# Optimization experiments

Hardware: AMD Instinct MI355X
Metric: run time of the kernel (lower is better)

Reference implementation:

```python
import jax, jax.numpy as jnp
import numpy as np

BETA = 20.0  # Softplus beta in the original torch module
# upper-triangular (offset=1) indices of a 3x3 matrix, matching torch.triu_indices(3,3,1)
TRIU_R = np.array([0, 0, 1])
TRIU_C = np.array([1, 2, 2])


def _softplus(x):
    # torch.nn.Softplus(beta=20): log(1+exp(beta*x))/beta, numerically stable via jax.nn.softplus
    return jax.nn.softplus(BETA * x) / BETA


def setup_inputs() -> dict:
    key = jax.random.key(0)
    ks = jax.random.split(key, 9)
    N = 1_000_000
    h = 32

    def lin_init(k, fan_in, fan_out):
        bound = 1.0 / np.sqrt(fan_in)
        kw, kb = jax.random.split(k)
        W = jax.random.uniform(kw, (fan_in, fan_out), jnp.float32, -bound, bound)
        b = jax.random.uniform(kb, (fan_out,), jnp.float32, -bound, bound)
        return W, b

    x = jax.random.normal(ks[0], (N, 3), jnp.float32)
    W1, b1 = lin_init(ks[1], 3, h)
    W2, b2 = lin_init(ks[2], h, h)
    W3, b3 = lin_init(ks[3], h, h)
    W4, b4 = lin_init(ks[4], h, 3)
    return {"x": x, "W1": W1, "b1": b1, "W2": W2, "b2": b2,
            "W3": W3, "b3": b3, "W4": W4, "b4": b4}


def reference(x, W1, b1, W2, b2, W3, b3, W4, b4):
    def mlp(p):  # p: [3] -> [3] (the 3 free entries of the antisymmetric matrix)
        h = _softplus(p @ W1 + b1)
        h = _softplus(h @ W2 + b2)
        h = _softplus(h @ W3 + b3)
        return h @ W4 + b4

    def pres_A(p):  # p: [3] -> antisymmetric [3,3]
        v = mlp(p)
        M = jnp.zeros((3, 3), dtype=p.dtype).at[TRIU_R, TRIU_C].set(v)
        return M - M.T

    # per-sample Jacobian dA/dx: [N, 3, 3, 3]
    J = jax.vmap(jax.jacrev(pres_A))(x.reshape(-1, 3))
    # trace over (column, x-dim): out[n, a] = sum_i dA[n, a, i]/dx[n, i]
    return jnp.einsum('naii->na', J)
```

## Files before the change

### kernel.cpp

```cpp
#include <hip/hip_runtime.h>
#include <math.h>

#define NTHR 256
#define WAVES_PER_BLOCK 4

typedef __attribute__((ext_vector_type(8))) _Float16 f16x8;
typedef __attribute__((ext_vector_type(2))) _Float16 half2v;
typedef __attribute__((ext_vector_type(4))) float f32x4;
typedef __attribute__((ext_vector_type(4))) unsigned uint4v;

#define CEXP 28.85390082f
#define KLOG 0.03465735903f

#define EXP2F(v) __builtin_amdgcn_exp2f(v)
#define LOG2F(v) __builtin_amdgcn_logf(v)

static __device__ __forceinline__ f32x4 splat4(float v) { return (f32x4){v, v, v, v}; }

static __device__ __forceinline__ void act_hs4(f32x4 z, f32x4& h, f32x4& s) {
    f32x4 az = __builtin_elementwise_abs(splat4(CEXP) * z);
    f32x4 e;
    #pragma unroll
    for (int i = 0; i < 4; ++i) e[i] = EXP2F(-az[i]);
    f32x4 p = splat4(1.0f) + e;
    f32x4 l;
    #pragma unroll
    for (int i = 0; i < 4; ++i) l[i] = LOG2F(p[i]);
    f32x4 zp = __builtin_elementwise_max(z, splat4(0.0f));
    f32x4 q  = __builtin_elementwise_fma(splat4(-CEXP), zp, -l);
    f32x4 t;
    #pragma unroll
    for (int i = 0; i < 4; ++i) t[i] = EXP2F(q[i]);
    s = splat4(1.0f) - t;
    h = __builtin_elementwise_fma(splat4(KLOG), l, zp);
}

static __device__ __forceinline__ f32x4 sigmoid4(f32x4 z) {
    f32x4 cz = splat4(-CEXP) * z;
    f32x4 e;
    #pragma unroll
    for (int i = 0; i < 4; ++i) e[i] = EXP2F(cz[i]);
    f32x4 p = splat4(1.0f) + e;
    f32x4 r;
    #pragma unroll
    for (int i = 0; i < 4; ++i) r[i] = __builtin_amdgcn_rcpf(p[i]);
    return r;
}

static __device__ __forceinline__ unsigned pk(float a, float b) {
    return __builtin_bit_cast(unsigned, __builtin_amdgcn_cvt_pkrtz(a, b));
}

static __device__ __forceinline__ f16x8 pack8v(const f32x4& a, const f32x4& b) {
    uint4v u = {pk(a[0], a[1]), pk(a[2], a[3]), pk(b[0], b[1]), pk(b[2], b[3])};
    return __builtin_bit_cast(f16x8, u);
}
static __device__ __forceinline__ void fsplit8v(const f32x4& a, const f32x4& b,
                                                f16x8& hi, f16x8& lo) {
    unsigned h[4], l[4];
    #pragma unroll
    for (int p2 = 0; p2 < 2; ++p2) {
        float u0 = a[2 * p2], u1 = a[2 * p2 + 1];
        unsigned hp = pk(u0, u1);
        half2v hh = __builtin_bit_cast(half2v, hp);
        h[p2] = hp;
        l[p2] = pk(u0 - (float)hh[0], u1 - (float)hh[1]);
        float w0 = b[2 * p2], w1 = b[2 * p2 + 1];
        unsigned hq = pk(w0, w1);
        half2v hh2 = __builtin_bit_cast(half2v, hq);
        h[2 + p2] = hq;
        l[2 + p2] = pk(w0 - (float)hh2[0], w1 - (float)hh2[1]);
    }
    hi = __builtin_bit_cast(f16x8, (uint4v){h[0], h[1], h[2], h[3]});
    lo = __builtin_bit_cast(f16x8, (uint4v){l[0], l[1], l[2], l[3]});
}

static __device__ __forceinline__ f32x4 mfma2f(f16x8 w, f16x8 bh, f16x8 bl, f32x4 c) {
    c = __builtin_amdgcn_mfma_f32_16x16x32_f16(w, bh, c, 0, 0, 0);
    c = __builtin_amdgcn_mfma_f32_16x16x32_f16(w, bl, c, 0, 0, 0);
    return c;
}
static __device__ __forceinline__ f32x4 mfma1t(f16x8 w, f16x8 b, f32x4 c) {
    return __builtin_amdgcn_mfma_f32_16x16x32_f16(w, b, c, 0, 0, 0);
}

__global__ void __launch_bounds__(NTHR)
presdiv_kernel(const float* __restrict__ x,
               const float* __restrict__ W1, const float* __restrict__ b1,
               const float* __restrict__ W2, const float* __restrict__ b2,
               const float* __restrict__ W3, const float* __restrict__ b3,
               const float* __restrict__ W4,
               float* __restrict__ out, int N)
{
    const int lane = threadIdx.x & 63;
    const int wid  = threadIdx.x >> 6;
    const int n16  = lane & 15;
    const int g    = lane >> 4;

    f16x8 w2[2], w3[2];
    #pragma unroll
    for (int h = 0; h < 2; ++h) {
        #pragma unroll
        for (int j = 0; j < 8; ++j) {
            const int k2 = g * 8 + j;
            w2[h][j] = (_Float16)W2[k2 * 32 + 16 * h + n16];
            const int k3 = (j < 4) ? (4 * g + j) : (16 + 4 * g + (j - 4));
            w3[h][j] = (_Float16)W3[k3 * 32 + 16 * h + n16];
        }
    }
    f32x4 w1v[3][2], bb1v[2];
    #pragma unroll
    for (int c = 0; c < 2; ++c)
        #pragma unroll
        for (int i = 0; i < 4; ++i) {
            const int j = 4 * c + i;
            bb1v[c][i] = b1[g * 8 + j];
            #pragma unroll
            for (int d = 0; d < 3; ++d) w1v[d][c][i] = W1[d * 32 + g * 8 + j];
        }
    f32x4 bb2v[2], bb3v[2], w4c[2][3];
    #pragma unroll
    for (int h = 0; h < 2; ++h)
        #pragma unroll
        for (int r = 0; r < 4; ++r) {
            const int row = 16 * h + 4 * g + r;
            bb2v[h][r] = b2[row];
            bb3v[h][r] = b3[row];
            #pragma unroll
            for (int k = 0; k < 3; ++k) w4c[h][k][r] = W4[row * 3 + k];
        }

    const int ntiles = (N + 15) >> 4;
    const int nwaves = gridDim.x * WAVES_PER_BLOCK;
    const f32x4 vzero = {0.f, 0.f, 0.f, 0.f};

    for (int tile = blockIdx.x * WAVES_PER_BLOCK + wid; tile < ntiles; tile += nwaves) {
        int s = tile * 16 + n16;
        if (s >= N) s = N - 1;
        const f32x4 X0 = splat4(x[3 * s + 0]);
        const f32x4 X1 = splat4(x[3 * s + 1]);
        const f32x4 X2 = splat4(x[3 * s + 2]);

        f32x4 vFv[2], v0v[2], v1v[2], v2v[2];
        #pragma unroll
        for (int c = 0; c < 2; ++c) {
            f32x4 z = __builtin_elementwise_fma(X0, w1v[0][c], bb1v[c]);
            z = __builtin_elementwise_fma(X1, w1v[1][c], z);
            z = __builtin_elementwise_fma(X2, w1v[2][c], z);
            f32x4 hv, sv;
            act_hs4(z, hv, sv);
            vFv[c] = hv;
            v0v[c] = sv * w1v[0][c];
            v1v[c] = sv * w1v[1][c];
            v2v[c] = sv * w1v[2][c];
        }

        f32x4 aF[2], a0[2], a1[2], a2[2];
        aF[0] = bb2v[0]; aF[1] = bb2v[1];
        a0[0] = a0[1] = a1[0] = a1[1] = a2[0] = a2[1] = vzero;

        f16x8 bh, bl;
        fsplit8v(vFv[0], vFv[1], bh, bl);
        aF[0] = mfma2f(w2[0], bh, bl, aF[0]);
        aF[1] = mfma2f(w2[1], bh, bl, aF[1]);
        f16x8 tb = pack8v(v0v[0], v0v[1]);
        a0[0] = mfma1t(w2[0], tb, a0[0]);
        a0[1] = mfma1t(w2[1], tb, a0[1]);
        tb = pack8v(v1v[0], v1v[1]);
        a1[0] = mfma1t(w2[0], tb, a1[0]);
        a1[1] = mfma1t(w2[1], tb, a1[1]);
        tb = pack8v(v2v[0], v2v[1]);
        a2[0] = mfma1t(w2[0], tb, a2[0]);
        a2[1] = mfma1t(w2[1], tb, a2[1]);

        #pragma unroll
        for (int h = 0; h < 2; ++h) {
            f32x4 hv, sv;
            act_hs4(aF[h], hv, sv);
            aF[h] = hv;
            a0[h] *= sv;
            a1[h] *= sv;
            a2[h] *= sv;
        }

        f32x4 zF[2], u0[2], u1[2], u2[2];
        zF[0] = bb3v[0]; zF[1] = bb3v[1];
        u0[0] = u0[1] = u1[0] = u1[1] = u2[0] = u2[1] = vzero;

        fsplit8v(aF[0], aF[1], bh, bl);
        zF[0] = mfma2f(w3[0], bh, bl, zF[0]);
        zF[1] = mfma2f(w3[1], bh, bl, zF[1]);
        tb = pack8v(a0[0], a0[1]);
        u0[0] = mfma1t(w3[0], tb, u0[0]);
        u0[1] = mfma1t(w3[1], tb, u0[1]);
        tb = pack8v(a1[0], a1[1]);
        u1[0] = mfma1t(w3[0], tb, u1[0]);
        u1[1] = mfma1t(w3[1], tb, u1[1]);
        tb = pack8v(a2[0], a2[1]);
        u2[0] = mfma1t(w3[0], tb, u2[0]);
        u2[1] = mfma1t(w3[1], tb, u2[1]);

        f32x4 O0 = vzero, O1 = vzero, O2 = vzero;
        #pragma unroll
        for (int h = 0; h < 2; ++h) {
            const f32x4 S  = sigmoid4(zF[h]);
            const f32x4 T0 = S * u0[h];
            const f32x4 T1 = S * u1[h];
            const f32x4 T2 = S * u2[h];
            O0 = __builtin_elementwise_fma(T1, w4c[h][0],
                 __builtin_elementwise_fma(T2, w4c[h][1], O0));
            O1 = __builtin_elementwise_fma(-T0, w4c[h][0],
                 __builtin_elementwise_fma(T2, w4c[h][2], O1));
            O2 = __builtin_elementwise_fma(-T0, w4c[h][1],
                 __builtin_elementwise_fma(-T1, w4c[h][2], O2));
        }
        float o0 = (O0[0] + O0[1]) + (O0[2] + O0[3]);
        float o1 = (O1[0] + O1[1]) + (O1[2] + O1[3]);
        float o2 = (O2[0] + O2[1]) + (O2[2] + O2[3]);

        o0 += __shfl_xor(o0, 16); o0 += __shfl_xor(o0, 32);
        o1 += __shfl_xor(o1, 16); o1 += __shfl_xor(o1, 32);
        o2 += __shfl_xor(o2, 16); o2 += __shfl_xor(o2, 32);

        if (g == 0) {
            out[3 * s + 0] = o0;
            out[3 * s + 1] = o1;
            out[3 * s + 2] = o2;
        }
    }
}

extern "C" void kernel_launch(void* const* d_in, const int* in_sizes, int n_in,
                              void* d_out, int out_size, void* d_ws, size_t ws_size,
                              hipStream_t stream)
{
    const float* x  = (const float*)d_in[0];
    const float* W1 = (const float*)d_in[1];
    const float* b1 = (const float*)d_in[2];
    const float* W2 = (const float*)d_in[3];
    const float* b2 = (const float*)d_in[4];
    const float* W3 = (const float*)d_in[5];
    const float* b3 = (const float*)d_in[6];
    const float* W4 = (const float*)d_in[7];
    float* out = (float*)d_out;

    const int N = in_sizes[0] / 3;
    presdiv_kernel<<<4096, NTHR, 0, stream>>>(x, W1, b1, W2, b2, W3, b3, W4, out, N);
}
```

Before: 137.6 us.

## Replace transcendental softplus/sigmoid with shared-memory lookup table interpolation

Builds a 1024-entry table in LDS holding log1p(exp(-|z|)) and sigmoid values, and replaces the exp2/log2/rcp sequences in the activation functions with linear interpolation from that table. The aim is to take load off the transcendental unit, which runs at reduced rate. In exchange it adds LDS gathers, which can hit bank conflicts, plus a per-block table build and a barrier. Accuracy depends on a 0.02 step in beta*|z|, with values clamped at the table end.

```diff
diff --git a/kernel.cpp b/kernel.cpp
--- a/kernel.cpp
+++ b/kernel.cpp
@@ -15,36 +15,50 @@
 #define EXP2F(v) __builtin_amdgcn_exp2f(v)
 #define LOG2F(v) __builtin_amdgcn_logf(v)
 
+#if __has_builtin(__builtin_amdgcn_fractf)
+#define FRACTF(v) __builtin_amdgcn_fractf(v)
+#else
+#define FRACTF(v) ((v) - floorf(v))
+#endif
+
+#define TBL_N    1024
+#define TBL_STEP 0.02f
+#define KIDX     1442.695041f
+#define TBL_MAX  1022.99f
+
 static __device__ __forceinline__ f32x4 splat4(float v) { return (f32x4){v, v, v, v}; }
 
-static __device__ __forceinline__ void act_hs4(f32x4 z, f32x4& h, f32x4& s) {
-    f32x4 az = __builtin_elementwise_abs(splat4(CEXP) * z);
-    f32x4 e;
-    #pragma unroll
-    for (int i = 0; i < 4; ++i) e[i] = EXP2F(-az[i]);
-    f32x4 p = splat4(1.0f) + e;
-    f32x4 l;
-    #pragma unroll
-    for (int i = 0; i < 4; ++i) l[i] = LOG2F(p[i]);
-    f32x4 zp = __builtin_elementwise_max(z, splat4(0.0f));
-    f32x4 q  = __builtin_elementwise_fma(splat4(-CEXP), zp, -l);
-    f32x4 t;
-    #pragma unroll
-    for (int i = 0; i < 4; ++i) t[i] = EXP2F(q[i]);
-    s = splat4(1.0f) - t;
-    h = __builtin_elementwise_fma(splat4(KLOG), l, zp);
-}
-
-static __device__ __forceinline__ f32x4 sigmoid4(f32x4 z) {
-    f32x4 cz = splat4(-CEXP) * z;
-    f32x4 e;
-    #pragma unroll
-    for (int i = 0; i < 4; ++i) e[i] = EXP2F(cz[i]);
-    f32x4 p = splat4(1.0f) + e;
-    f32x4 r;
-    #pragma unroll
-    for (int i = 0; i < 4; ++i) r[i] = __builtin_amdgcn_rcpf(p[i]);
-    return r;
+static __device__ __forceinline__ void act_lut4(const float2* __restrict__ t,
+                                                f32x4 z, f32x4& h, f32x4& s) {
+    #pragma unroll
+    for (int i = 0; i < 4; ++i) {
+        const float zi = z[i];
+        float m = fminf(fabsf(zi) * KIDX, TBL_MAX);
+        const unsigned j = (unsigned)m;
+        const float f = FRACTF(m);
+        const float2 ea = t[j];
+        const float2 eb = t[j + 1];
+        const float l  = fmaf(f, eb.x - ea.x, ea.x);
+        const float sm = fmaf(f, eb.y - ea.y, ea.y);
+        h[i] = fmaxf(zi, 0.0f) + l;
+        s[i] = 0.5f + copysignf(sm - 0.5f, zi);
+    }
+}
+
+static __device__ __forceinline__ f32x4 sig_lut4(const float2* __restrict__ t, f32x4 z) {
+    f32x4 s;
+    #pragma unroll
+    for (int i = 0; i < 4; ++i) {
+        const float zi = z[i];
+        float m = fminf(fabsf(zi) * KIDX, TBL_MAX);
+        const unsigned j = (unsigned)m;
+        const float f = FRACTF(m);
+        const float sa = t[j].y;
+        const float sb = t[j + 1].y;
+        const float sm = fmaf(f, sb - sa, sa);
+        s[i] = 0.5f + copysignf(sm - 0.5f, zi);
+    }
+    return s;
 }
 
 static __device__ __forceinline__ unsigned pk(float a, float b) {
@@ -92,6 +106,16 @@
                const float* __restrict__ W4,
                float* __restrict__ out, int N)
 {
+    __shared__ float2 s_tbl[TBL_N];
+
+    for (int j = threadIdx.x; j < TBL_N; j += NTHR) {
+        const float az = (float)j * TBL_STEP;
+        const float e  = EXP2F(-az);
+        const float p  = 1.0f + e;
+        s_tbl[j] = make_float2(KLOG * LOG2F(p), 1.0f / p);
+    }
+    __syncthreads();
+
     const int lane = threadIdx.x & 63;
     const int wid  = threadIdx.x >> 6;
     const int n16  = lane & 15;
@@ -148,7 +172,7 @@
             z = __builtin_elementwise_fma(X1, w1v[1][c], z);
             z = __builtin_elementwise_fma(X2, w1v[2][c], z);
             f32x4 hv, sv;
-            act_hs4(z, hv, sv);
+            act_lut4(s_tbl, z, hv, sv);
             vFv[c] = hv;
             v0v[c] = sv * w1v[0][c];
             v1v[c] = sv * w1v[1][c];
@@ -176,7 +200,7 @@
         #pragma unroll
         for (int h = 0; h < 2; ++h) {
             f32x4 hv, sv;
-            act_hs4(aF[h], hv, sv);
+            act_lut4(s_tbl, aF[h], hv, sv);
             aF[h] = hv;
             a0[h] *= sv;
             a1[h] *= sv;
@@ -203,7 +227,7 @@
         f32x4 O0 = vzero, O1 = vzero, O2 = vzero;
         #pragma unroll
         for (int h = 0; h < 2; ++h) {
-            const f32x4 S  = sigmoid4(zF[h]);
+            const f32x4 S  = sig_lut4(s_tbl, zF[h]);
             const f32x4 T0 = S * u0[h];
             const f32x4 T1 = S * u1[h];
             const f32x4 T2 = S * u2[h];
```

Result: slower. 150.2 us (+9.2%).
